# Kernel tuning notes

Measured on AMD Instinct MI355X. Metric: run time of the kernel, lower is better.

## Reference

```python
import jax, jax.numpy as jnp
import numpy as np

D_MODEL, D_STATE, B, S = 1024, 64, 8, 2048


def setup_inputs() -> dict:
    key = jax.random.key(0)
    ks = jax.random.split(key, 14)
    inp = {"x": jax.random.normal(ks[0], (B, S, D_MODEL), jnp.float32)}
    names = ["cog", "beh", "env", "delta", "Bp", "Cp"]
    for i, n in enumerate(names):
        inp[f"W_{n}"] = jax.random.normal(ks[1 + 2 * i], (D_STATE, D_MODEL), jnp.float32) / np.sqrt(D_MODEL)
        inp[f"b_{n}"] = jnp.zeros((D_STATE,), jnp.float32)
    # torch init is log(|randn|+1e-4); we use strictly-negative A_log so the
    # length-2048 multiplicative recurrence stays finite (A_log is a learned
    # parameter, so its value is free; the math of forward is unchanged).
    inp["A_log"] = -jnp.abs(jax.random.normal(ks[13], (D_STATE, D_STATE), jnp.float32)) - 0.1
    return inp


def reference(x, W_cog, b_cog, W_beh, b_beh, W_env, b_env,
              W_delta, b_delta, W_Bp, b_Bp, W_Cp, b_Cp, A_log):
    # gating terms (computed in the source but never used downstream)
    A_t = (jax.nn.sigmoid(x @ W_cog.T + b_cog)
           * jax.nn.sigmoid(x @ W_beh.T + b_beh)
           * jax.nn.sigmoid(x @ W_env.T + b_env))
    del A_t

    delta = jax.nn.softplus(x @ W_delta.T + b_delta)   # [B,S,N]
    Bt = x @ W_Bp.T + b_Bp                             # [B,S,N]
    Ct = x @ W_Cp.T + b_Cp                             # [B,S,N]
    u = Bt * x[:, :, :D_STATE]                         # [B,S,N]

    # Faithful to torch broadcasting: after step 0 the carried state h is
    # [B,N,N] with h[b,i,j] = exp(A_log[i,j]*delta[b,t,i]) * h_prev[b,i,j] + u[b,t,j]
    def step(h, td):
        d, u_t, c_t = td                               # each [B,N]
        A = jnp.exp(A_log[None, :, :] * d[:, :, None]) # [B,N,N]
        h = A * h + u_t[:, None, :]
        y = jnp.einsum('bj,bij->bi', c_t, h)           # [B,N]
        return h, y

    h0 = jnp.zeros((x.shape[0], D_STATE, D_STATE), x.dtype)
    _, ys = jax.lax.scan(
        step, h0,
        (delta.transpose(1, 0, 2), u.transpose(1, 0, 2), Ct.transpose(1, 0, 2)))
    # torch stacks y_t of shape [B,1,N] along dim=1 -> [B,S,1,N]
    return ys.transpose(1, 0, 2)[:, :, None, :]
```

## Files before the change

### kernel.cpp

```cpp
#include <hip/hip_runtime.h>
#include <math.h>

#define DM   1024
#define DS   64
#define BATCH 8
#define SEQ  2048
#define CL   32
#define NC   64

typedef __bf16 bf16x8 __attribute__((ext_vector_type(8)));
typedef float  f32x4  __attribute__((ext_vector_type(4)));

#if __has_builtin(__builtin_amdgcn_exp2f)
#define EXP2(v) __builtin_amdgcn_exp2f(v)
#else
#define EXP2(v) __expf(0.69314718056f * (v))
#endif

__global__ __launch_bounds__(256) void wconv_kernel(
    const float* __restrict__ Wd, const float* __restrict__ Wb,
    const float* __restrict__ Wc, __bf16* __restrict__ Wp)
{
    int idx = blockIdx.x * 256 + threadIdx.x;
    int k  = idx & 1023;
    int n  = idx >> 10;
    const float* W = (n < 64) ? Wd : (n < 128 ? Wb : Wc);
    float v = W[(size_t)(n & 63) * DM + k];
    int kt = k >> 5, kk = k & 31;
    Wp[((size_t)kt * 192 + n) * 32 + kk] = (__bf16)v;
}

__global__ __launch_bounds__(256, 2) void proj_mfma(
    const float* __restrict__ x, const __bf16* __restrict__ Wp,
    const float* __restrict__ bd, const float* __restrict__ bb,
    const float* __restrict__ bc,
    float* __restrict__ delta_g, float* __restrict__ u_g,
    float* __restrict__ ct_g)
{
    __shared__ __bf16 sB[2][12288];
    __shared__ __bf16 sA[2][32 * 72];

    const int tid  = threadIdx.x;
    const int row0 = blockIdx.x * 32;

    const int lane = tid & 63, wv = tid >> 6;
    const int l15  = lane & 15, quad = lane >> 4;
    const int nbase = wv * 48;

    const int am = tid >> 3;
    const int ak = tid & 7;
    const float* xga = x + (size_t)(row0 + am) * DM + ak * 8;

    f32x4 acc[2][3];
    #pragma unroll
    for (int mt = 0; mt < 2; ++mt)
        #pragma unroll
        for (int nt = 0; nt < 3; ++nt)
            acc[mt][nt] = (f32x4){0.f, 0.f, 0.f, 0.f};

    uint4  wreg[6];
    float4 areg[2];

    #define LOADB(kb) do {                                                    \
        _Pragma("unroll")                                                     \
        for (int it = 0; it < 6; ++it)                                        \
            wreg[it] = *(const uint4*)(                                       \
                Wp + (size_t)(kb) * 12288 + (tid + it * 256) * 8);            \
    } while (0)
    #define LOADA(kb) do {                                                    \
        areg[0] = *(const float4*)(xga + (kb) * 64);                          \
        areg[1] = *(const float4*)(xga + (kb) * 64 + 4);                      \
    } while (0)
    #define STAGE(bi) do {                                                    \
        _Pragma("unroll")                                                     \
        for (int it = 0; it < 6; ++it)                                        \
            *(uint4*)&sB[bi][(tid + it * 256) * 8] = wreg[it];                \
        bf16x8 hv = {(__bf16)areg[0].x, (__bf16)areg[0].y,                    \
                     (__bf16)areg[0].z, (__bf16)areg[0].w,                    \
                     (__bf16)areg[1].x, (__bf16)areg[1].y,                    \
                     (__bf16)areg[1].z, (__bf16)areg[1].w};                   \
        *(bf16x8*)&sA[bi][am * 72 + ak * 8] = hv;                             \
    } while (0)
    #define COMPUTE(bi) do {                                                  \
        _Pragma("unroll")                                                     \
        for (int s = 0; s < 2; ++s) {                                         \
            bf16x8 af[2];                                                     \
            _Pragma("unroll")                                                 \
            for (int mt = 0; mt < 2; ++mt)                                    \
                af[mt] = *(const bf16x8*)                                     \
                    &sA[bi][(mt * 16 + l15) * 72 + s * 32 + quad * 8];        \
            _Pragma("unroll")                                                 \
            for (int nt = 0; nt < 3; ++nt) {                                  \
                bf16x8 bv = *(const bf16x8*)                                  \
                    &sB[bi][s * 6144 + (nbase + nt * 16 + l15) * 32           \
                            + quad * 8];                                      \
                _Pragma("unroll")                                             \
                for (int mt = 0; mt < 2; ++mt)                                \
                    acc[mt][nt] = __builtin_amdgcn_mfma_f32_16x16x32_bf16(    \
                        af[mt], bv, acc[mt][nt], 0, 0, 0);                    \
            }                                                                 \
        }                                                                     \
    } while (0)

    LOADB(0);
    LOADA(0);
    STAGE(0);
    __syncthreads();

    int buf = 0;
    for (int kb = 0; kb < 16; ++kb) {
        if (kb < 15) {
            LOADB(kb + 1);
            LOADA(kb + 1);
        }
        COMPUTE(buf);
        if (kb < 15) STAGE(buf ^ 1);
        __syncthreads();
        buf ^= 1;
    }
    #undef LOADB
    #undef LOADA
    #undef STAGE
    #undef COMPUTE

    #pragma unroll
    for (int nt = 0; nt < 3; ++nt) {
        int gn  = nbase + nt * 16 + l15;
        int mat = (nbase + nt * 16) >> 6;
        int col = gn & 63;
        float bias = (mat == 0) ? bd[col] : (mat == 1 ? bb[col] : bc[col]);
        #pragma unroll
        for (int mt = 0; mt < 2; ++mt) {
            #pragma unroll
            for (int r = 0; r < 4; ++r) {
                int m = row0 + mt * 16 + quad * 4 + r;
                float v = acc[mt][nt][r] + bias;
                if (mat == 0) {
                    float sp = (v > 20.f) ? v : __logf(1.f + __expf(v));
                    delta_g[(size_t)m * DS + col] = sp;
                } else if (mat == 1) {
                    u_g[(size_t)m * DS + col] = v * x[(size_t)m * DM + col];
                } else {
                    ct_g[(size_t)m * DS + col] = v;
                }
            }
        }
    }
}

__global__ __launch_bounds__(256) void pass1_kernel(
    const float* __restrict__ delta_g, const float* __restrict__ u_g,
    const float* __restrict__ A_log,
    float* __restrict__ E, float* __restrict__ Dsum)
{
    __shared__ float s_d[CL * 64];
    __shared__ float s_u[CL * 64];
    const int c = blockIdx.x, b = blockIdx.y, tid = threadIdx.x;
    const int t0 = c * CL;

    const float4* dg = (const float4*)(delta_g + ((size_t)b * SEQ + t0) * DS);
    const float4* ug = (const float4*)(u_g     + ((size_t)b * SEQ + t0) * DS);
    #pragma unroll
    for (int it = 0; it < (CL * 64 / 4) / 256; ++it) {
        int f = tid + it * 256;
        ((float4*)s_d)[f] = dg[f];
        ((float4*)s_u)[f] = ug[f];
    }

    const int i  = tid & 63;
    const int jg = tid >> 6;
    float alog[16];
    {
        const float4* ar = (const float4*)(A_log + i * 64 + jg * 16);
        #pragma unroll
        for (int qq = 0; qq < 4; ++qq) {
            float4 v = ar[qq];
            alog[4*qq+0] = v.x * 1.44269504f; alog[4*qq+1] = v.y * 1.44269504f;
            alog[4*qq+2] = v.z * 1.44269504f; alog[4*qq+3] = v.w * 1.44269504f;
        }
    }
    __syncthreads();

    float h[16];
    #pragma unroll
    for (int k = 0; k < 16; ++k) h[k] = 0.f;
    float dsum = 0.f;

    for (int t = 0; t < CL; ++t) {
        float d = s_d[t * 64 + i];
        dsum += d;
        const float* up = s_u + t * 64 + jg * 16;
        #pragma unroll
        for (int k = 0; k < 16; ++k)
            h[k] = EXP2(alog[k] * d) * h[k] + up[k];
    }

    float* eo = E + (((size_t)c * BATCH + b) * 64 + i) * 64 + jg * 16;
    #pragma unroll
    for (int qq = 0; qq < 4; ++qq)
        ((float4*)eo)[qq] = make_float4(h[4*qq], h[4*qq+1], h[4*qq+2], h[4*qq+3]);
    if (jg == 0) Dsum[((size_t)c * BATCH + b) * 64 + i] = dsum;
}

__global__ __launch_bounds__(256) void pass2_kernel(
    const float* __restrict__ A_log, const float* __restrict__ E,
    const float* __restrict__ Dsum, float* __restrict__ Sin)
{
    const int g = blockIdx.x * 256 + threadIdx.x;
    const int b = g >> 12;
    const int e = g & 4095;
    const int i = e >> 6;
    const float al = A_log[e] * 1.44269504f;

    float Eb[8], db[8];
    #pragma unroll
    for (int p = 0; p < 8; ++p) {
        size_t nb = (size_t)p * BATCH + b;
        Eb[p] = E[nb * 4096 + e];
        db[p] = EXP2(al * Dsum[nb * 64 + i]);
    }

    float carry = 0.f;
    #pragma unroll 8
    for (int c = 0; c < NC; ++c) {
        const int s = c & 7;
        float Ec = Eb[s], dc = db[s];
        if (c + 8 < NC) {
            size_t nb = (size_t)(c + 8) * BATCH + b;
            Eb[s] = E[nb * 4096 + e];
            db[s] = EXP2(al * Dsum[nb * 64 + i]);
        }
        Sin[((size_t)c * BATCH + b) * 4096 + e] = carry;
        carry = dc * carry + Ec;
    }
}

__global__ __launch_bounds__(256) void pass3_kernel(
    const float* __restrict__ delta_g, const float* __restrict__ u_g,
    const float* __restrict__ ct_g, const float* __restrict__ A_log,
    const float* __restrict__ Sin, float* __restrict__ out)
{
    __shared__ float s_d[CL * 64];
    __shared__ float s_u[CL * 64];
    __shared__ float s_c[CL * 64];

    const int c = blockIdx.x, b = blockIdx.y, tid = threadIdx.x;
    const int t0 = c * CL;

    const float4* dg = (const float4*)(delta_g + ((size_t)b * SEQ + t0) * DS);
    const float4* ug = (const float4*)(u_g     + ((size_t)b * SEQ + t0) * DS);
    const float4* cg = (const float4*)(ct_g    + ((size_t)b * SEQ + t0) * DS);
    #pragma unroll
    for (int it = 0; it < (CL * 64 / 4) / 256; ++it) {
        int f = tid + it * 256;
        ((float4*)s_d)[f] = dg[f];
        ((float4*)s_u)[f] = ug[f];
        ((float4*)s_c)[f] = cg[f];
    }

    const int i  = tid >> 2;
    const int jg = tid & 3;

    float alog[16];
    {
        const float4* ar = (const float4*)(A_log + i * 64 + jg * 16);
        #pragma unroll
        for (int qq = 0; qq < 4; ++qq) {
            float4 v = ar[qq];
            alog[4*qq+0] = v.x * 1.44269504f; alog[4*qq+1] = v.y * 1.44269504f;
            alog[4*qq+2] = v.z * 1.44269504f; alog[4*qq+3] = v.w * 1.44269504f;
        }
    }

    float h[16];
    {
        const float4* hin = (const float4*)(
            Sin + (((size_t)c * BATCH + b) * 64 + i) * 64 + jg * 16);
        #pragma unroll
        for (int qq = 0; qq < 4; ++qq) {
            float4 v = hin[qq];
            h[4*qq+0] = v.x; h[4*qq+1] = v.y; h[4*qq+2] = v.z; h[4*qq+3] = v.w;
        }
    }
    __syncthreads();

    for (int t = 0; t < CL; ++t) {
        float d = s_d[t * 64 + i];
        const float* up = s_u + t * 64 + jg * 16;
        const float* cp = s_c + t * 64 + jg * 16;
        float part = 0.f;
        #pragma unroll
        for (int k = 0; k < 16; ++k) {
            h[k] = EXP2(alog[k] * d) * h[k] + up[k];
            part += cp[k] * h[k];
        }
        part += __shfl_xor(part, 1);
        part += __shfl_xor(part, 2);
        if (jg == 0)
            out[((size_t)b * SEQ + t0 + t) * DS + i] = part;
    }
}

extern "C" void kernel_launch(void* const* d_in, const int* in_sizes, int n_in,
                              void* d_out, int out_size, void* d_ws, size_t ws_size,
                              hipStream_t stream)
{
    const float* x     = (const float*)d_in[0];
    const float* Wd    = (const float*)d_in[7];
    const float* bd    = (const float*)d_in[8];
    const float* Wb    = (const float*)d_in[9];
    const float* bb    = (const float*)d_in[10];
    const float* Wc    = (const float*)d_in[11];
    const float* bc    = (const float*)d_in[12];
    const float* A_log = (const float*)d_in[13];
    float* out = (float*)d_out;

    float* ws = (float*)d_ws;
    float* delta_g = ws;
    float* u_g     = ws + 1 * 1048576;
    float* ct_g    = ws + 2 * 1048576;
    float* E       = ws + 3 * 1048576;
    float* Sin     = ws + 5 * 1048576;
    float* Dsum    = ws + 7 * 1048576;
    __bf16* Wp     = (__bf16*)E;

    wconv_kernel<<<768, 256, 0, stream>>>(Wd, Wb, Wc, Wp);
    proj_mfma<<<512, 256, 0, stream>>>(
        x, Wp, bd, bb, bc, delta_g, u_g, ct_g);
    pass1_kernel<<<dim3(NC, BATCH), 256, 0, stream>>>(
        delta_g, u_g, A_log, E, Dsum);
    pass2_kernel<<<128, 256, 0, stream>>>(
        A_log, E, Dsum, Sin);
    pass3_kernel<<<dim3(NC, BATCH), 256, 0, stream>>>(
        delta_g, u_g, ct_g, A_log, Sin, out);
}
```

Measured before the change: 186.9 us.

## Fuse chunk-local scan into projection and fold carry propagation into final pass

The projection kernel now also runs the pass-1 chunk scan from shared-memory copies of delta and u, so those values are not re-read from global memory in a separate launch. The pass-2 carry kernel is removed: each pass-3 block recomputes its incoming state by serially combining all earlier chunk summaries, which costs O(chunks) extra work on later chunks. Weight tiles are loaded straight into LDS with global_load_lds when that builtin exists. Together these cut two kernel launches and the Sin buffer, at the cost of load imbalance in the final pass.

Result: no change. 186.0 us (-0.5%).

```diff
diff --git a/kernel.cpp b/kernel.cpp
--- a/kernel.cpp
+++ b/kernel.cpp
@@ -30,15 +30,18 @@
     Wp[((size_t)kt * 192 + n) * 32 + kk] = (__bf16)v;
 }
 
-__global__ __launch_bounds__(256, 2) void proj_mfma(
+__global__ __launch_bounds__(256, 2) void projp1_full(
     const float* __restrict__ x, const __bf16* __restrict__ Wp,
     const float* __restrict__ bd, const float* __restrict__ bb,
-    const float* __restrict__ bc,
+    const float* __restrict__ bc, const float* __restrict__ A_log,
     float* __restrict__ delta_g, float* __restrict__ u_g,
-    float* __restrict__ ct_g)
+    float* __restrict__ ct_g,
+    float* __restrict__ E, float* __restrict__ Dsum)
 {
     __shared__ __bf16 sB[2][12288];
     __shared__ __bf16 sA[2][32 * 72];
+    __shared__ float  s_d[CL * 64];
+    __shared__ float  s_u[CL * 64];
 
     const int tid  = threadIdx.x;
     const int row0 = blockIdx.x * 32;
@@ -58,23 +61,35 @@
         for (int nt = 0; nt < 3; ++nt)
             acc[mt][nt] = (f32x4){0.f, 0.f, 0.f, 0.f};
 
-    uint4  wreg[6];
     float4 areg[2];
 
-    #define LOADB(kb) do {                                                    \
+#if __has_builtin(__builtin_amdgcn_global_load_lds)
+    #define LOADB(kb, bi) do {                                                \
         _Pragma("unroll")                                                     \
-        for (int it = 0; it < 6; ++it)                                        \
-            wreg[it] = *(const uint4*)(                                       \
+        for (int it = 0; it < 6; ++it) {                                      \
+            const __bf16* gsrc =                                              \
+                Wp + (size_t)(kb) * 12288 + (tid + it * 256) * 8;             \
+            __bf16* ldst = &sB[bi][(tid + it * 256) * 8];                     \
+            __builtin_amdgcn_global_load_lds(                                 \
+                (const __attribute__((address_space(1))) void*)gsrc,          \
+                (__attribute__((address_space(3))) void*)ldst, 16, 0, 0);     \
+        }                                                                     \
+    } while (0)
+#else
+    #define LOADB(kb, bi) do {                                                \
+        _Pragma("unroll")                                                     \
+        for (int it = 0; it < 6; ++it) {                                      \
+            uint4 t = *(const uint4*)(                                        \
                 Wp + (size_t)(kb) * 12288 + (tid + it * 256) * 8);            \
-    } while (0)
+            *(uint4*)&sB[bi][(tid + it * 256) * 8] = t;                       \
+        }                                                                     \
+    } while (0)
+#endif
     #define LOADA(kb) do {                                                    \
         areg[0] = *(const float4*)(xga + (kb) * 64);                          \
         areg[1] = *(const float4*)(xga + (kb) * 64 + 4);                      \
     } while (0)
-    #define STAGE(bi) do {                                                    \
-        _Pragma("unroll")                                                     \
-        for (int it = 0; it < 6; ++it)                                        \
-            *(uint4*)&sB[bi][(tid + it * 256) * 8] = wreg[it];                \
+    #define STAGEA(bi) do {                                                   \
         bf16x8 hv = {(__bf16)areg[0].x, (__bf16)areg[0].y,                    \
                      (__bf16)areg[0].z, (__bf16)areg[0].w,                    \
                      (__bf16)areg[1].x, (__bf16)areg[1].y,                    \
@@ -102,25 +117,25 @@
         }                                                                     \
     } while (0)
 
-    LOADB(0);
+    LOADB(0, 0);
     LOADA(0);
-    STAGE(0);
+    STAGEA(0);
     __syncthreads();
 
     int buf = 0;
     for (int kb = 0; kb < 16; ++kb) {
         if (kb < 15) {
-            LOADB(kb + 1);
+            LOADB(kb + 1, buf ^ 1);
             LOADA(kb + 1);
         }
         COMPUTE(buf);
-        if (kb < 15) STAGE(buf ^ 1);
+        if (kb < 15) STAGEA(buf ^ 1);
         __syncthreads();
         buf ^= 1;
     }
     #undef LOADB
     #undef LOADA
-    #undef STAGE
+    #undef STAGEA
     #undef COMPUTE
 
     #pragma unroll
@@ -133,45 +148,33 @@
         for (int mt = 0; mt < 2; ++mt) {
             #pragma unroll
             for (int r = 0; r < 4; ++r) {
-                int m = row0 + mt * 16 + quad * 4 + r;
+                int tl = mt * 16 + quad * 4 + r;
+                int m  = row0 + tl;
                 float v = acc[mt][nt][r] + bias;
                 if (mat == 0) {
                     float sp = (v > 20.f) ? v : __logf(1.f + __expf(v));
                     delta_g[(size_t)m * DS + col] = sp;
+                    s_d[tl * 64 + col] = sp;
                 } else if (mat == 1) {
-                    u_g[(size_t)m * DS + col] = v * x[(size_t)m * DM + col];
+                    float uu = v * x[(size_t)m * DM + col];
+                    u_g[(size_t)m * DS + col] = uu;
+                    s_u[tl * 64 + col] = uu;
                 } else {
                     ct_g[(size_t)m * DS + col] = v;
                 }
             }
         }
     }
-}
-
-__global__ __launch_bounds__(256) void pass1_kernel(
-    const float* __restrict__ delta_g, const float* __restrict__ u_g,
-    const float* __restrict__ A_log,
-    float* __restrict__ E, float* __restrict__ Dsum)
-{
-    __shared__ float s_d[CL * 64];
-    __shared__ float s_u[CL * 64];
-    const int c = blockIdx.x, b = blockIdx.y, tid = threadIdx.x;
-    const int t0 = c * CL;
-
-    const float4* dg = (const float4*)(delta_g + ((size_t)b * SEQ + t0) * DS);
-    const float4* ug = (const float4*)(u_g     + ((size_t)b * SEQ + t0) * DS);
-    #pragma unroll
-    for (int it = 0; it < (CL * 64 / 4) / 256; ++it) {
-        int f = tid + it * 256;
-        ((float4*)s_d)[f] = dg[f];
-        ((float4*)s_u)[f] = ug[f];
-    }
-
-    const int i  = tid & 63;
-    const int jg = tid >> 6;
+    __syncthreads();
+
+    const int bidx = row0 >> 11;
+    const int cidx = (row0 >> 5) & 63;
+    const int si = tid & 63;
+    const int sj = tid >> 6;
+
     float alog[16];
     {
-        const float4* ar = (const float4*)(A_log + i * 64 + jg * 16);
+        const float4* ar = (const float4*)(A_log + si * 64 + sj * 16);
         #pragma unroll
         for (int qq = 0; qq < 4; ++qq) {
             float4 v = ar[qq];
@@ -179,7 +182,6 @@
             alog[4*qq+2] = v.z * 1.44269504f; alog[4*qq+3] = v.w * 1.44269504f;
         }
     }
-    __syncthreads();
 
     float h[16];
     #pragma unroll
@@ -187,58 +189,26 @@
     float dsum = 0.f;
 
     for (int t = 0; t < CL; ++t) {
-        float d = s_d[t * 64 + i];
+        float d = s_d[t * 64 + si];
         dsum += d;
-        const float* up = s_u + t * 64 + jg * 16;
+        const float* up = s_u + t * 64 + sj * 16;
         #pragma unroll
         for (int k = 0; k < 16; ++k)
             h[k] = EXP2(alog[k] * d) * h[k] + up[k];
     }
 
-    float* eo = E + (((size_t)c * BATCH + b) * 64 + i) * 64 + jg * 16;
+    float* eo = E + (((size_t)cidx * BATCH + bidx) * 64 + si) * 64 + sj * 16;
     #pragma unroll
     for (int qq = 0; qq < 4; ++qq)
         ((float4*)eo)[qq] = make_float4(h[4*qq], h[4*qq+1], h[4*qq+2], h[4*qq+3]);
-    if (jg == 0) Dsum[((size_t)c * BATCH + b) * 64 + i] = dsum;
+    if (sj == 0) Dsum[((size_t)cidx * BATCH + bidx) * 64 + si] = dsum;
 }
 
-__global__ __launch_bounds__(256) void pass2_kernel(
-    const float* __restrict__ A_log, const float* __restrict__ E,
-    const float* __restrict__ Dsum, float* __restrict__ Sin)
-{
-    const int g = blockIdx.x * 256 + threadIdx.x;
-    const int b = g >> 12;
-    const int e = g & 4095;
-    const int i = e >> 6;
-    const float al = A_log[e] * 1.44269504f;
-
-    float Eb[8], db[8];
-    #pragma unroll
-    for (int p = 0; p < 8; ++p) {
-        size_t nb = (size_t)p * BATCH + b;
-        Eb[p] = E[nb * 4096 + e];
-        db[p] = EXP2(al * Dsum[nb * 64 + i]);
-    }
-
-    float carry = 0.f;
-    #pragma unroll 8
-    for (int c = 0; c < NC; ++c) {
-        const int s = c & 7;
-        float Ec = Eb[s], dc = db[s];
-        if (c + 8 < NC) {
-            size_t nb = (size_t)(c + 8) * BATCH + b;
-            Eb[s] = E[nb * 4096 + e];
-            db[s] = EXP2(al * Dsum[nb * 64 + i]);
-        }
-        Sin[((size_t)c * BATCH + b) * 4096 + e] = carry;
-        carry = dc * carry + Ec;
-    }
-}
-
-__global__ __launch_bounds__(256) void pass3_kernel(
+__global__ __launch_bounds__(256) void pass23_kernel(
     const float* __restrict__ delta_g, const float* __restrict__ u_g,
     const float* __restrict__ ct_g, const float* __restrict__ A_log,
-    const float* __restrict__ Sin, float* __restrict__ out)
+    const float* __restrict__ E, const float* __restrict__ Dsum,
+    float* __restrict__ out)
 {
     __shared__ float s_d[CL * 64];
     __shared__ float s_u[CL * 64];
@@ -273,26 +243,31 @@
     }
 
     float h[16];
-    {
-        const float4* hin = (const float4*)(
-            Sin + (((size_t)c * BATCH + b) * 64 + i) * 64 + jg * 16);
-        #pragma unroll
-        for (int qq = 0; qq < 4; ++qq) {
-            float4 v = hin[qq];
-            h[4*qq+0] = v.x; h[4*qq+1] = v.y; h[4*qq+2] = v.z; h[4*qq+3] = v.w;
-        }
+    #pragma unroll
+    for (int k = 0; k < 16; ++k) h[k] = 0.f;
+
+    for (int cp = 0; cp < c; ++cp) {
+        float ds = Dsum[((size_t)cp * BATCH + b) * 64 + i];
+        const float4* ep = (const float4*)(
+            E + (((size_t)cp * BATCH + b) * 64 + i) * 64 + jg * 16);
+        float4 e0 = ep[0], e1 = ep[1], e2 = ep[2], e3 = ep[3];
+        float ev[16] = {e0.x,e0.y,e0.z,e0.w, e1.x,e1.y,e1.z,e1.w,
+                        e2.x,e2.y,e2.z,e2.w, e3.x,e3.y,e3.z,e3.w};
+        #pragma unroll
+        for (int k = 0; k < 16; ++k)
+            h[k] = EXP2(alog[k] * ds) * h[k] + ev[k];
     }
     __syncthreads();
 
     for (int t = 0; t < CL; ++t) {
         float d = s_d[t * 64 + i];
-        const float* up = s_u + t * 64 + jg * 16;
-        const float* cp = s_c + t * 64 + jg * 16;
+        const float* up  = s_u + t * 64 + jg * 16;
+        const float* cp2 = s_c + t * 64 + jg * 16;
         float part = 0.f;
         #pragma unroll
         for (int k = 0; k < 16; ++k) {
             h[k] = EXP2(alog[k] * d) * h[k] + up[k];
-            part += cp[k] * h[k];
+            part += cp2[k] * h[k];
         }
         part += __shfl_xor(part, 1);
         part += __shfl_xor(part, 2);
@@ -320,17 +295,12 @@
     float* u_g     = ws + 1 * 1048576;
     float* ct_g    = ws + 2 * 1048576;
     float* E       = ws + 3 * 1048576;
-    float* Sin     = ws + 5 * 1048576;
-    float* Dsum    = ws + 7 * 1048576;
-    __bf16* Wp     = (__bf16*)E;
+    float* Dsum    = ws + 5 * 1048576;
+    __bf16* Wp     = (__bf16*)(ws + 5 * 1048576 + 65536);
 
     wconv_kernel<<<768, 256, 0, stream>>>(Wd, Wb, Wc, Wp);
-    proj_mfma<<<512, 256, 0, stream>>>(
-        x, Wp, bd, bb, bc, delta_g, u_g, ct_g);
-    pass1_kernel<<<dim3(NC, BATCH), 256, 0, stream>>>(
-        delta_g, u_g, A_log, E, Dsum);
-    pass2_kernel<<<128, 256, 0, stream>>>(
-        A_log, E, Dsum, Sin);
-    pass3_kernel<<<dim3(NC, BATCH), 256, 0, stream>>>(
-        delta_g, u_g, ct_g, A_log, Sin, out);
+    projp1_full<<<512, 256, 0, stream>>>(
+        x, Wp, bd, bb, bc, A_log, delta_g, u_g, ct_g, E, Dsum);
+    pass23_kernel<<<dim3(NC, BATCH), 256, 0, stream>>>(
+        delta_g, u_g, ct_g, A_log, E, Dsum, out);
 }
```

## Split projection across N halves with direct-to-LDS loads; checkpoint pass2 carries every 8 chunks

Applied to the files above, without the earlier changes.

The projection GEMM is split into two N-halves per row tile with 128-thread blocks, and the weight tiles are loaded with global_load_lds so they bypass registers. The chunk-scan pass2 now stores carry state only every 8 chunks instead of every chunk. Pass3 rebuilds its starting state from the nearest checkpoint by replaying up to 7 chunk summaries (E, Dsum) itself. This cuts pass2's write traffic and Sin storage, at the cost of redundant recompute and extra E reads in pass3, and it doubles the x reads in the projection.

Measured after the change: 200.9 us. +7.5%, slower.

```diff
diff --git a/kernel.cpp b/kernel.cpp
--- a/kernel.cpp
+++ b/kernel.cpp
@@ -30,26 +30,26 @@
     Wp[((size_t)kt * 192 + n) * 32 + kk] = (__bf16)v;
 }
 
-__global__ __launch_bounds__(256, 2) void proj_mfma(
+__global__ __launch_bounds__(128, 2) void proj_kernel(
     const float* __restrict__ x, const __bf16* __restrict__ Wp,
     const float* __restrict__ bd, const float* __restrict__ bb,
     const float* __restrict__ bc,
     float* __restrict__ delta_g, float* __restrict__ u_g,
     float* __restrict__ ct_g)
 {
-    __shared__ __bf16 sB[2][12288];
+    __shared__ __bf16 sB[2][6144];
     __shared__ __bf16 sA[2][32 * 72];
 
     const int tid  = threadIdx.x;
     const int row0 = blockIdx.x * 32;
+    const int nh   = blockIdx.y;
 
     const int lane = tid & 63, wv = tid >> 6;
     const int l15  = lane & 15, quad = lane >> 4;
-    const int nbase = wv * 48;
-
-    const int am = tid >> 3;
-    const int ak = tid & 7;
-    const float* xga = x + (size_t)(row0 + am) * DM + ak * 8;
+
+    const int am = tid >> 2;
+    const int ak = tid & 3;
+    const float* xga = x + (size_t)(row0 + am) * DM + ak * 16;
 
     f32x4 acc[2][3];
     #pragma unroll
@@ -58,28 +58,54 @@
         for (int nt = 0; nt < 3; ++nt)
             acc[mt][nt] = (f32x4){0.f, 0.f, 0.f, 0.f};
 
-    uint4  wreg[6];
-    float4 areg[2];
-
-    #define LOADB(kb) do {                                                    \
+    float4 areg[4];
+
+#if __has_builtin(__builtin_amdgcn_global_load_lds)
+    #define LOADB(kb, bi) do {                                                \
         _Pragma("unroll")                                                     \
-        for (int it = 0; it < 6; ++it)                                        \
-            wreg[it] = *(const uint4*)(                                       \
-                Wp + (size_t)(kb) * 12288 + (tid + it * 256) * 8);            \
-    } while (0)
+        for (int it = 0; it < 6; ++it) {                                      \
+            int g   = tid + it * 128;                                         \
+            int ktl = (it >= 3) ? 1 : 0;                                      \
+            int r   = g - ktl * 384;                                          \
+            const __bf16* gsrc = Wp +                                         \
+                ((size_t)((kb) * 2 + ktl) * 192 + nh * 96 + (r >> 2)) * 32    \
+                + (r & 3) * 8;                                                \
+            __bf16* ldst = &sB[bi][g * 8];                                    \
+            __builtin_amdgcn_global_load_lds(                                 \
+                (const __attribute__((address_space(1))) void*)gsrc,          \
+                (__attribute__((address_space(3))) void*)ldst, 16, 0, 0);     \
+        }                                                                     \
+    } while (0)
+#else
+    #define LOADB(kb, bi) do {                                                \
+        _Pragma("unroll")                                                     \
+        for (int it = 0; it < 6; ++it) {                                      \
+            int g   = tid + it * 128;                                         \
+            int ktl = (it >= 3) ? 1 : 0;                                      \
+            int r   = g - ktl * 384;                                          \
+            uint4 t = *(const uint4*)(Wp +                                    \
+                ((size_t)((kb) * 2 + ktl) * 192 + nh * 96 + (r >> 2)) * 32    \
+                + (r & 3) * 8);                                               \
+            *(uint4*)&sB[bi][g * 8] = t;                                      \
+        }                                                                     \
+    } while (0)
+#endif
     #define LOADA(kb) do {                                                    \
-        areg[0] = *(const float4*)(xga + (kb) * 64);                          \
-        areg[1] = *(const float4*)(xga + (kb) * 64 + 4);                      \
-    } while (0)
-    #define STAGE(bi) do {                                                    \
         _Pragma("unroll")                                                     \
-        for (int it = 0; it < 6; ++it)                                        \
-            *(uint4*)&sB[bi][(tid + it * 256) * 8] = wreg[it];                \
-        bf16x8 hv = {(__bf16)areg[0].x, (__bf16)areg[0].y,                    \
+        for (int p = 0; p < 4; ++p)                                           \
+            areg[p] = *(const float4*)(xga + (kb) * 64 + p * 4);              \
+    } while (0)
+    #define STAGEA(bi) do {                                                   \
+        bf16x8 h0 = {(__bf16)areg[0].x, (__bf16)areg[0].y,                    \
                      (__bf16)areg[0].z, (__bf16)areg[0].w,                    \
                      (__bf16)areg[1].x, (__bf16)areg[1].y,                    \
                      (__bf16)areg[1].z, (__bf16)areg[1].w};                   \
-        *(bf16x8*)&sA[bi][am * 72 + ak * 8] = hv;                             \
+        bf16x8 h1 = {(__bf16)areg[2].x, (__bf16)areg[2].y,                    \
+                     (__bf16)areg[2].z, (__bf16)areg[2].w,                    \
+                     (__bf16)areg[3].x, (__bf16)areg[3].y,                    \
+                     (__bf16)areg[3].z, (__bf16)areg[3].w};                   \
+        *(bf16x8*)&sA[bi][am * 72 + ak * 16] = h0;                            \
+        *(bf16x8*)&sA[bi][am * 72 + ak * 16 + 8] = h1;                        \
     } while (0)
     #define COMPUTE(bi) do {                                                  \
         _Pragma("unroll")                                                     \
@@ -92,7 +118,7 @@
             _Pragma("unroll")                                                 \
             for (int nt = 0; nt < 3; ++nt) {                                  \
                 bf16x8 bv = *(const bf16x8*)                                  \
-                    &sB[bi][s * 6144 + (nbase + nt * 16 + l15) * 32           \
+                    &sB[bi][s * 3072 + (wv * 48 + nt * 16 + l15) * 32         \
                             + quad * 8];                                      \
                 _Pragma("unroll")                                             \
                 for (int mt = 0; mt < 2; ++mt)                                \
@@ -102,32 +128,33 @@
         }                                                                     \
     } while (0)
 
-    LOADB(0);
+    LOADB(0, 0);
     LOADA(0);
-    STAGE(0);
+    STAGEA(0);
     __syncthreads();
 
     int buf = 0;
     for (int kb = 0; kb < 16; ++kb) {
         if (kb < 15) {
-            LOADB(kb + 1);
+            LOADB(kb + 1, buf ^ 1);
             LOADA(kb + 1);
         }
         COMPUTE(buf);
-        if (kb < 15) STAGE(buf ^ 1);
+        if (kb < 15) STAGEA(buf ^ 1);
         __syncthreads();
         buf ^= 1;
     }
     #undef LOADB
     #undef LOADA
-    #undef STAGE
+    #undef STAGEA
     #undef COMPUTE
 
     #pragma unroll
     for (int nt = 0; nt < 3; ++nt) {
-        int gn  = nbase + nt * 16 + l15;
-        int mat = (nbase + nt * 16) >> 6;
-        int col = gn & 63;
+        int nwin = nh * 96 + wv * 48 + nt * 16;
+        int gn   = nwin + l15;
+        int mat  = nwin >> 6;
+        int col  = gn & 63;
         float bias = (mat == 0) ? bd[col] : (mat == 1 ? bb[col] : bc[col]);
         #pragma unroll
         for (int mt = 0; mt < 2; ++mt) {
@@ -202,9 +229,9 @@
     if (jg == 0) Dsum[((size_t)c * BATCH + b) * 64 + i] = dsum;
 }
 
-__global__ __launch_bounds__(256) void pass2_kernel(
+__global__ __launch_bounds__(256) void pass2ck_kernel(
     const float* __restrict__ A_log, const float* __restrict__ E,
-    const float* __restrict__ Dsum, float* __restrict__ Sin)
+    const float* __restrict__ Dsum, float* __restrict__ Sck)
 {
     const int g = blockIdx.x * 256 + threadIdx.x;
     const int b = g >> 12;
@@ -230,15 +257,17 @@
             Eb[s] = E[nb * 4096 + e];
             db[s] = EXP2(al * Dsum[nb * 64 + i]);
         }
-        Sin[((size_t)c * BATCH + b) * 4096 + e] = carry;
+        if (c > 0 && (c & 7) == 0)
+            Sck[(((size_t)(c >> 3) - 1) * BATCH + b) * 4096 + e] = carry;
         carry = dc * carry + Ec;
     }
 }
 
-__global__ __launch_bounds__(256) void pass3_kernel(
+__global__ __launch_bounds__(256) void pass3ck_kernel(
     const float* __restrict__ delta_g, const float* __restrict__ u_g,
     const float* __restrict__ ct_g, const float* __restrict__ A_log,
-    const float* __restrict__ Sin, float* __restrict__ out)
+    const float* __restrict__ E, const float* __restrict__ Dsum,
+    const float* __restrict__ Sck, float* __restrict__ out)
 {
     __shared__ float s_d[CL * 64];
     __shared__ float s_u[CL * 64];
@@ -260,6 +289,7 @@
 
     const int i  = tid >> 2;
     const int jg = tid & 3;
+    const int e  = i * 64 + jg * 16;
 
     float alog[16];
     {
@@ -273,26 +303,41 @@
     }
 
     float h[16];
-    {
-        const float4* hin = (const float4*)(
-            Sin + (((size_t)c * BATCH + b) * 64 + i) * 64 + jg * 16);
-        #pragma unroll
-        for (int qq = 0; qq < 4; ++qq) {
-            float4 v = hin[qq];
-            h[4*qq+0] = v.x; h[4*qq+1] = v.y; h[4*qq+2] = v.z; h[4*qq+3] = v.w;
-        }
+    #pragma unroll
+    for (int k = 0; k < 16; ++k) h[k] = 0.f;
+
+    if (c >= 8) {
+        const float4* sp = (const float4*)(
+            Sck + (((size_t)(c >> 3) - 1) * BATCH + b) * 4096 + e);
+        float4 s0 = sp[0], s1 = sp[1], s2 = sp[2], s3 = sp[3];
+        h[0]=s0.x; h[1]=s0.y; h[2]=s0.z; h[3]=s0.w;
+        h[4]=s1.x; h[5]=s1.y; h[6]=s1.z; h[7]=s1.w;
+        h[8]=s2.x; h[9]=s2.y; h[10]=s2.z; h[11]=s2.w;
+        h[12]=s3.x; h[13]=s3.y; h[14]=s3.z; h[15]=s3.w;
+    }
+    const int c0 = c & ~7;
+    for (int cp = c0; cp < c; ++cp) {
+        float ds = Dsum[((size_t)cp * BATCH + b) * 64 + i];
+        const float4* ep = (const float4*)(
+            E + ((size_t)cp * BATCH + b) * 4096 + e);
+        float4 e0 = ep[0], e1 = ep[1], e2 = ep[2], e3 = ep[3];
+        float ev[16] = {e0.x,e0.y,e0.z,e0.w, e1.x,e1.y,e1.z,e1.w,
+                        e2.x,e2.y,e2.z,e2.w, e3.x,e3.y,e3.z,e3.w};
+        #pragma unroll
+        for (int k = 0; k < 16; ++k)
+            h[k] = EXP2(alog[k] * ds) * h[k] + ev[k];
     }
     __syncthreads();
 
     for (int t = 0; t < CL; ++t) {
         float d = s_d[t * 64 + i];
-        const float* up = s_u + t * 64 + jg * 16;
-        const float* cp = s_c + t * 64 + jg * 16;
+        const float* up  = s_u + t * 64 + jg * 16;
+        const float* cp2 = s_c + t * 64 + jg * 16;
         float part = 0.f;
         #pragma unroll
         for (int k = 0; k < 16; ++k) {
             h[k] = EXP2(alog[k] * d) * h[k] + up[k];
-            part += cp[k] * h[k];
+            part += cp2[k] * h[k];
         }
         part += __shfl_xor(part, 1);
         part += __shfl_xor(part, 2);
@@ -320,17 +365,17 @@
     float* u_g     = ws + 1 * 1048576;
     float* ct_g    = ws + 2 * 1048576;
     float* E       = ws + 3 * 1048576;
-    float* Sin     = ws + 5 * 1048576;
-    float* Dsum    = ws + 7 * 1048576;
-    __bf16* Wp     = (__bf16*)E;
+    float* Dsum    = ws + 5 * 1048576;
+    float* Sck     = ws + 5 * 1048576 + 65536;
+    __bf16* Wp     = (__bf16*)(ws + 6 * 1048576);
 
     wconv_kernel<<<768, 256, 0, stream>>>(Wd, Wb, Wc, Wp);
-    proj_mfma<<<512, 256, 0, stream>>>(
+    proj_kernel<<<dim3(512, 2), 128, 0, stream>>>(
         x, Wp, bd, bb, bc, delta_g, u_g, ct_g);
     pass1_kernel<<<dim3(NC, BATCH), 256, 0, stream>>>(
         delta_g, u_g, A_log, E, Dsum);
-    pass2_kernel<<<128, 256, 0, stream>>>(
-        A_log, E, Dsum, Sin);
-    pass3_kernel<<<dim3(NC, BATCH), 256, 0, stream>>>(
-        delta_g, u_g, ct_g, A_log, Sin, out);
-}
+    pass2ck_kernel<<<128, 256, 0, stream>>>(
+        A_log, E, Dsum, Sck);
+    pass3ck_kernel<<<dim3(NC, BATCH), 256, 0, stream>>>(
+        delta_g, u_g, ct_g, A_log, E, Dsum, Sck, out);
+}
```
